# Performance work log

Hardware: AMD Instinct MI355X
Metric: run time of the kernel (lower is better)

Reference implementation:

```python
import math
import jax, jax.numpy as jnp
import numpy as np

MUL = 16          # multiplicity of 0e and 1o in irreps_in/out
DIM = 4 * MUL     # 16 scalars + 16 vectors*3 = 64 channels
DIAMETER = 5.0
STEPS = (1.0, 1.0, 1.0)
NB = 8            # num_radial_basis


def gen_lattice():
    r = DIAMETER / 2
    ax = [jnp.arange(-math.floor(r / s), math.floor(r / s) + 1.0) * s for s in STEPS]
    return jnp.stack(jnp.meshgrid(*ax, indexing='ij'), axis=-1)  # [kx,ky,kz,3]


def radial_emb(r):
    # soft_one_hot_linspace(basis='smooth_finite', cutoff=True)
    values = jnp.linspace(0.0, DIAMETER / 2, NB + 2)[1:-1]
    step = (DIAMETER / 2) / (NB + 1)
    diff = (r[..., None] - values) / step
    den = jnp.maximum(1.0 - diff * diff, 1e-9)  # avoid nan grads outside support
    return jnp.where(jnp.abs(diff) < 1.0, 1.14136 * jnp.exp(2.0 - 1.0 / den), 0.0)


def sph_l01(vec):
    # spherical harmonics l=0,1 with normalize=True, normalization='component'
    n = jnp.linalg.norm(vec, axis=-1, keepdims=True)
    unit = jnp.where(n > 0, vec / jnp.where(n > 0, n, 1.0), 0.0)
    y0 = jnp.ones(vec.shape[:-1] + (1,), vec.dtype)
    return jnp.concatenate([y0, math.sqrt(3.0) * unit], axis=-1)  # [...,4]


def tp_right(w, sh):
    # Right operand of fully-connected tensor product (in x sh -> out):
    # returns per-lattice-point matrix R [L, DIM_in, DIM_out] s.t. TP(x, sh) = x @ R.
    # Paths (uvw): 0e*0e->0e, 0e*1o->1o, 1o*0e->1o, 1o*1o->0e.
    L = w.shape[0]
    W = w.reshape(L, 4, MUL, MUL)      # per-path weights [u, w] (mul_sh = 1)
    y0, y1 = sh[:, 0], sh[:, 1:4]
    a = 1.0 / math.sqrt(2.0 * MUL)     # fan-in: mul_in * mul_sh * 2 paths per output
    eye3 = jnp.eye(3, dtype=w.dtype)
    Rss = a * W[:, 0] * y0[:, None, None]                                            # [L,16,16]
    Rsv = a * jnp.einsum('luw,lm->luwm', W[:, 1], y1).reshape(L, MUL, 3 * MUL)        # CG = identity
    Rvv = a * jnp.einsum('luw,l,mn->lumwn', W[:, 2], y0, eye3).reshape(L, 3 * MUL, 3 * MUL)
    Rvs = (a / math.sqrt(3.0)) * jnp.einsum('luw,lm->lumw', W[:, 3], y1).reshape(L, 3 * MUL, MUL)  # CG = delta/sqrt3
    return jnp.concatenate([jnp.concatenate([Rss, Rsv], -1),
                            jnp.concatenate([Rvs, Rvv], -1)], 1)  # [L,64,64]


def reference(x, linear_weight, weight):
    lattice = gen_lattice()
    emb = radial_emb(jnp.linalg.norm(lattice, axis=-1))   # [kx,ky,kz,NB]
    sh = sph_l01(lattice)                                  # [kx,ky,kz,4]
    # self-connection: irrep-wise Linear with 1/sqrt(fan_in)
    Wl = linear_weight.reshape(2, MUL, MUL) / math.sqrt(MUL)
    xs = x[..., :MUL]
    xv = x[..., MUL:].reshape(x.shape[:-1] + (MUL, 3))
    sc = jnp.concatenate([
        jnp.einsum('...u,uw->...w', xs, Wl[0]),
        jnp.einsum('...um,uw->...wm', xv, Wl[1]).reshape(x.shape[:-1] + (3 * MUL,))], -1)
    # radial-MLP weights -> per-voxel TP kernel
    kx, ky, kz = sh.shape[:3]
    w = (emb.reshape(-1, NB) @ weight) / (kx * ky * kz)    # [L, 4*MUL*MUL]
    k = tp_right(w, sh.reshape(-1, 4)).reshape(kx, ky, kz, DIM, DIM)
    y = jax.lax.conv_general_dilated(x, k, (1, 1, 1), 'SAME',
                                     dimension_numbers=('NXYZC', 'XYZIO', 'NXYZC'))
    return sc + y


def setup_inputs():
    key = jax.random.key(0)
    k1, k2, k3 = jax.random.split(key, 3)
    return {
        'x': jax.random.normal(k1, (2, 40, 40, 40, DIM), jnp.float32),
        'linear_weight': jax.random.normal(k2, (2 * MUL * MUL,), jnp.float32),
        'weight': jax.random.normal(k3, (NB, 4 * MUL * MUL), jnp.float32),
    }
```

## Files before the change

### kernel.cpp

```cpp
#include <hip/hip_runtime.h>
#include <hip/hip_bf16.h>


typedef __bf16 bf16x8 __attribute__((ext_vector_type(8)));
typedef float f32x4 __attribute__((ext_vector_type(4)));

#define COLCH 577
#define COLSTRIDE (COLCH * 16)
#define LDS_BYTES (8 * COLSTRIDE)

__global__ __launch_bounds__(256) void build_k(const float* __restrict__ lw,
                                               const float* __restrict__ wt,
                                               ushort* __restrict__ Kb) {
  int tid = blockIdx.x * 256 + threadIdx.x;
  int j  = tid & 7;
  int o  = (tid >> 3) & 63;
  int kg = (tid >> 9) & 7;
  int l  = tid >> 12;
  int i  = kg * 8 + j;

  int ix = l / 25; int rem = l - ix * 25; int iy = rem / 5; int iz = rem - iy * 5;
  float cx = (float)(ix - 2), cy = (float)(iy - 2), cz = (float)(iz - 2);
  float r = sqrtf(cx * cx + cy * cy + cz * cz);

  float e[8];
  const float step = 2.5f / 9.0f;
  #pragma unroll
  for (int b = 0; b < 8; b++) {
    float diff = (r - (float)(b + 1) * step) / step;
    float den = fmaxf(1.0f - diff * diff, 1e-9f);
    e[b] = (fabsf(diff) < 1.0f) ? 1.14136f * expf(2.0f - 1.0f / den) : 0.0f;
  }
  float inv = (r > 0.0f) ? 1.0f / r : 0.0f;
  const float s3 = 1.7320508075688772f;
  float y1[3] = { s3 * cx * inv, s3 * cy * inv, s3 * cz * inv };
  const float a  = 0.17677669529663687f;
  const float a3 = 0.10206207261596575f;

  auto wElem = [&](int c, int u, int w) -> float {
    const float* p = wt + c * 256 + u * 16 + w;
    float s = 0.f;
    #pragma unroll
    for (int b = 0; b < 8; b++) s += e[b] * p[b * 1024];
    return s * (1.0f / 125.0f);
  };

  float val;
  if (i < 16) {
    if (o < 16) {
      val = a * wElem(0, i, o);
    } else {
      int om = o - 16; int w = om / 3, m = om - 3 * w;
      val = a * wElem(1, i, w) * y1[m];
    }
  } else {
    int im = i - 16; int u = im / 3, m = im - 3 * u;
    if (o < 16) {
      val = a3 * wElem(3, u, o) * y1[m];
    } else {
      int om = o - 16; int w = om / 3, nn = om - 3 * w;
      val = (m == nn) ? a * wElem(2, u, w) : 0.0f;
    }
  }
  if (l == 62) {
    if (i < 16 && o < 16) {
      val += lw[i * 16 + o] * 0.25f;
    } else if (i >= 16 && o >= 16) {
      int im = i - 16, om = o - 16;
      int u = im / 3, m = im - 3 * u;
      int w = om / 3, nn = om - 3 * w;
      if (m == nn) val += lw[256 + u * 16 + w] * 0.25f;
    }
  }
  __hip_bfloat16 h = __float2bfloat16(val);
  Kb[tid] = *(ushort*)&h;
}

__global__ __launch_bounds__(256, 2) void conv_mfma(const float* __restrict__ x,
                                                    const ushort* __restrict__ Kb_,
                                                    float* __restrict__ out) {
  const char* KbB = (const char*)Kb_;
  __shared__ __align__(16) char smem[LDS_BYTES];

  const int tid = threadIdx.x;
  const int lane = tid & 63;
  const int wv = tid >> 6;
  const int g = lane >> 4, ol = lane & 15;

  int bid = blockIdx.x;
  int yg = bid % 5; int t = bid / 5;
  int ox = t % 40; int n = t / 40;
  int y0 = yg * 8;
  int p0 = ((n * 40 + ox) * 40 + y0) * 40;

  int lanebase[5];
  #pragma unroll
  for (int mt = 0; mt < 5; mt++) {
    int r = wv * 80 + mt * 16 + ol;
    int oyr = r / 40, oz = r - oyr * 40;
    lanebase[mt] = g * COLSTRIDE + (oyr * 48 + oz) * 16;
  }
  const int bbase = g * 1024 + ol * 16;

  f32x4 acc[5][4] = {};

  const float* xn = x + (size_t)n * 40 * 40 * 40 * 64;

  for (int dx = 0; dx < 5; dx++) {
    int ix = ox + dx - 2;
    if (ix < 0 || ix >= 40) continue;
    __syncthreads();
    const float* xpl = xn + (size_t)ix * 40 * 40 * 64;
    for (int it = 0; it < 17; it++) {
      int c = it * 256 + tid;
      if (c < 4224) {
        int ch8 = c & 7;
        int rowsrc = c >> 3;
        int yrel = rowsrc / 44;
        int zr = rowsrc - yrel * 44;
        int iy = y0 - 2 + yrel;
        int iz = zr - 2;
        int4 st = make_int4(0, 0, 0, 0);
        if (iy >= 0 && iy < 40 && iz >= 0 && iz < 40) {
          const float* src = xpl + ((size_t)iy * 40 + iz) * 64 + ch8 * 8;
          float4 f0 = ((const float4*)src)[0];
          float4 f1 = ((const float4*)src)[1];
          union { __hip_bfloat16 h[8]; int4 v4; } u;
          u.h[0] = __float2bfloat16(f0.x); u.h[1] = __float2bfloat16(f0.y);
          u.h[2] = __float2bfloat16(f0.z); u.h[3] = __float2bfloat16(f0.w);
          u.h[4] = __float2bfloat16(f1.x); u.h[5] = __float2bfloat16(f1.y);
          u.h[6] = __float2bfloat16(f1.z); u.h[7] = __float2bfloat16(f1.w);
          st = u.v4;
        }
        *(int4*)(smem + ch8 * COLSTRIDE + (yrel * 48 + zr) * 16) = st;
      }
    }
    __syncthreads();

    const char* kbdx = KbB + (size_t)dx * 25 * 8192 + bbase;
    #pragma unroll 1
    for (int dy = 0; dy < 5; dy++) {
      const int dyoff = dy * 48 * 16;
      const char* kbdy = kbdx + dy * 5 * 8192;
      #pragma unroll
      for (int dz = 0; dz < 5; dz++) {
        const int toff = dyoff + dz * 16;
        bf16x8 a[5][2], b[2][4];
        #pragma unroll
        for (int mt = 0; mt < 5; mt++)
          #pragma unroll
          for (int kc = 0; kc < 2; kc++)
            a[mt][kc] = *(const bf16x8*)(smem + lanebase[mt] + kc * (4 * COLSTRIDE) + toff);
        const char* kb = kbdy + dz * 8192;
        #pragma unroll
        for (int kc = 0; kc < 2; kc++)
          #pragma unroll
          for (int nt = 0; nt < 4; nt++)
            b[kc][nt] = *(const bf16x8*)(kb + kc * 4096 + nt * 256);
        #pragma unroll
        for (int kc = 0; kc < 2; kc++)
          #pragma unroll
          for (int nt = 0; nt < 4; nt++)
            #pragma unroll
            for (int mt = 0; mt < 5; mt++)
              acc[mt][nt] = __builtin_amdgcn_mfma_f32_16x16x32_bf16(a[mt][kc], b[kc][nt], acc[mt][nt], 0, 0, 0);
      }
    }
  }

  __syncthreads();
  float* sw = (float*)(smem + wv * (16 * 66 * 4));
  #pragma unroll 1
  for (int mt = 0; mt < 5; mt++) {
    #pragma unroll
    for (int nt = 0; nt < 4; nt++)
      #pragma unroll
      for (int j = 0; j < 4; j++)
        sw[(g * 4 + j) * 66 + nt * 16 + ol] = acc[mt][nt][j];
    float* outb = out + (size_t)(p0 + wv * 80 + mt * 16) * 64;
    #pragma unroll
    for (int i = 0; i < 4; i++) {
      int4 vv = *(int4*)&sw[(i * 4 + g) * 66 + ol * 4];
      ((int4*)outb)[i * 64 + lane] = vv;
    }
  }
}

extern "C" void kernel_launch(void* const* d_in, const int* in_sizes, int n_in,
                              void* d_out, int out_size, void* d_ws, size_t ws_size,
                              hipStream_t stream) {
  const float* x  = (const float*)d_in[0];
  const float* lw = (const float*)d_in[1];
  const float* wt = (const float*)d_in[2];
  float* out = (float*)d_out;
  ushort* Kb = (ushort*)d_ws;

  build_k<<<2000, 256, 0, stream>>>(lw, wt, Kb);
  conv_mfma<<<400, 256, 0, stream>>>(x, Kb, out);
}
```

Baseline: 301.1 us.

## Pre-pad and convert input to bf16 halves, split conv into smaller blocks

A prep kernel now writes a zero-padded bf16 copy of x, split into two 32-channel halves, alongside the fused kernel-weight build. The conv kernel loads slabs straight from this buffer with no bounds checks or fp32 conversion, and loops over channel halves to halve LDS usage. It runs 800 blocks of 128 threads with an XCD-aware block remap. Output is written directly from registers instead of being staged through LDS. The cost is an extra global round trip for the padded bf16 copy and output stores that are less coalesced.

```diff
diff --git a/kernel.cpp b/kernel.cpp
--- a/kernel.cpp
+++ b/kernel.cpp
@@ -5,80 +5,109 @@
 typedef __bf16 bf16x8 __attribute__((ext_vector_type(8)));
 typedef float f32x4 __attribute__((ext_vector_type(4)));
 
-#define COLCH 577
-#define COLSTRIDE (COLCH * 16)
-#define LDS_BYTES (8 * COLSTRIDE)
+#define XP_CHUNKS 1362944
+#define XP_BYTES  (XP_CHUNKS * 16)
+#define COLU 385
+#define COLSTRIDE (COLU * 16)
+#define LDS_BYTES (4 * COLSTRIDE)
 
-__global__ __launch_bounds__(256) void build_k(const float* __restrict__ lw,
-                                               const float* __restrict__ wt,
-                                               ushort* __restrict__ Kb) {
-  int tid = blockIdx.x * 256 + threadIdx.x;
-  int j  = tid & 7;
-  int o  = (tid >> 3) & 63;
-  int kg = (tid >> 9) & 7;
-  int l  = tid >> 12;
-  int i  = kg * 8 + j;
+__global__ __launch_bounds__(256) void prep(const float* __restrict__ x,
+                                            const float* __restrict__ lw,
+                                            const float* __restrict__ wt,
+                                            ushort* __restrict__ xp,
+                                            ushort* __restrict__ Kb) {
+  if (blockIdx.x < 5324) {
+    int u = blockIdx.x * 256 + threadIdx.x;
+    int c8 = u & 3;
+    int v = u >> 2;
+    int zi = v % 44; int w = v / 44;
+    int yi = w % 44; int w2 = w / 44;
+    int h = w2 & 1; int w3 = w2 >> 1;
+    int xi = w3 % 44; int n = w3 / 44;
+    int4 st = make_int4(0, 0, 0, 0);
+    if (xi >= 2 && xi < 42 && yi >= 2 && yi < 42 && zi >= 2 && zi < 42) {
+      const float* src = x + ((((size_t)n * 40 + (xi - 2)) * 40 + (yi - 2)) * 40 + (zi - 2)) * 64
+                           + h * 32 + c8 * 8;
+      float4 f0 = ((const float4*)src)[0];
+      float4 f1 = ((const float4*)src)[1];
+      union { __hip_bfloat16 hh[8]; int4 v4; } uu;
+      uu.hh[0] = __float2bfloat16(f0.x); uu.hh[1] = __float2bfloat16(f0.y);
+      uu.hh[2] = __float2bfloat16(f0.z); uu.hh[3] = __float2bfloat16(f0.w);
+      uu.hh[4] = __float2bfloat16(f1.x); uu.hh[5] = __float2bfloat16(f1.y);
+      uu.hh[6] = __float2bfloat16(f1.z); uu.hh[7] = __float2bfloat16(f1.w);
+      st = uu.v4;
+    }
+    ((int4*)xp)[u] = st;
+  } else {
+    int tid = (blockIdx.x - 5324) * 256 + threadIdx.x;
+    int j  = tid & 7;
+    int o  = (tid >> 3) & 63;
+    int kg = (tid >> 9) & 7;
+    int l  = tid >> 12;
+    int i  = kg * 8 + j;
 
-  int ix = l / 25; int rem = l - ix * 25; int iy = rem / 5; int iz = rem - iy * 5;
-  float cx = (float)(ix - 2), cy = (float)(iy - 2), cz = (float)(iz - 2);
-  float r = sqrtf(cx * cx + cy * cy + cz * cz);
+    int ix = l / 25; int rem = l - ix * 25; int iy = rem / 5; int iz = rem - iy * 5;
+    float cx = (float)(ix - 2), cy = (float)(iy - 2), cz = (float)(iz - 2);
+    float r = sqrtf(cx * cx + cy * cy + cz * cz);
 
-  float e[8];
-  const float step = 2.5f / 9.0f;
-  #pragma unroll
-  for (int b = 0; b < 8; b++) {
-    float diff = (r - (float)(b + 1) * step) / step;
-    float den = fmaxf(1.0f - diff * diff, 1e-9f);
-    e[b] = (fabsf(diff) < 1.0f) ? 1.14136f * expf(2.0f - 1.0f / den) : 0.0f;
+    float e[8];
+    const float step = 2.5f / 9.0f;
+    #pragma unroll
+    for (int b = 0; b < 8; b++) {
+      float diff = (r - (float)(b + 1) * step) / step;
+      float den = fmaxf(1.0f - diff * diff, 1e-9f);
+      e[b] = (fabsf(diff) < 1.0f) ? 1.14136f * expf(2.0f - 1.0f / den) : 0.0f;
+    }
+    float inv = (r > 0.0f) ? 1.0f / r : 0.0f;
+    const float s3 = 1.7320508075688772f;
+    float y1[3] = { s3 * cx * inv, s3 * cy * inv, s3 * cz * inv };
+    const float a  = 0.17677669529663687f;
+    const float a3 = 0.10206207261596575f;
+
+    auto wElem = [&](int c, int u_, int w_) -> float {
+      const float* p = wt + c * 256 + u_ * 16 + w_;
+      float s = 0.f;
+      #pragma unroll
+      for (int b = 0; b < 8; b++) s += e[b] * p[b * 1024];
+      return s * (1.0f / 125.0f);
+    };
+
+    float val;
+    if (i < 16) {
+      if (o < 16) {
+        val = a * wElem(0, i, o);
+      } else {
+        int om = o - 16; int w_ = om / 3, m = om - 3 * w_;
+        val = a * wElem(1, i, w_) * y1[m];
+      }
+    } else {
+      int im = i - 16; int u_ = im / 3, m = im - 3 * u_;
+      if (o < 16) {
+        val = a3 * wElem(3, u_, o) * y1[m];
+      } else {
+        int om = o - 16; int w_ = om / 3, nn = om - 3 * w_;
+        val = (m == nn) ? a * wElem(2, u_, w_) : 0.0f;
+      }
+    }
+    if (l == 62) {
+      if (i < 16 && o < 16) {
+        val += lw[i * 16 + o] * 0.25f;
+      } else if (i >= 16 && o >= 16) {
+        int im = i - 16, om = o - 16;
+        int u_ = im / 3, m = im - 3 * u_;
+        int w_ = om / 3, nn = om - 3 * w_;
+        if (m == nn) val += lw[256 + u_ * 16 + w_] * 0.25f;
+      }
+    }
+    __hip_bfloat16 hv = __float2bfloat16(val);
+    Kb[tid] = *(ushort*)&hv;
   }
-  float inv = (r > 0.0f) ? 1.0f / r : 0.0f;
-  const float s3 = 1.7320508075688772f;
-  float y1[3] = { s3 * cx * inv, s3 * cy * inv, s3 * cz * inv };
-  const float a  = 0.17677669529663687f;
-  const float a3 = 0.10206207261596575f;
-
-  auto wElem = [&](int c, int u, int w) -> float {
-    const float* p = wt + c * 256 + u * 16 + w;
-    float s = 0.f;
-    #pragma unroll
-    for (int b = 0; b < 8; b++) s += e[b] * p[b * 1024];
-    return s * (1.0f / 125.0f);
-  };
-
-  float val;
-  if (i < 16) {
-    if (o < 16) {
-      val = a * wElem(0, i, o);
-    } else {
-      int om = o - 16; int w = om / 3, m = om - 3 * w;
-      val = a * wElem(1, i, w) * y1[m];
-    }
-  } else {
-    int im = i - 16; int u = im / 3, m = im - 3 * u;
-    if (o < 16) {
-      val = a3 * wElem(3, u, o) * y1[m];
-    } else {
-      int om = o - 16; int w = om / 3, nn = om - 3 * w;
-      val = (m == nn) ? a * wElem(2, u, w) : 0.0f;
-    }
-  }
-  if (l == 62) {
-    if (i < 16 && o < 16) {
-      val += lw[i * 16 + o] * 0.25f;
-    } else if (i >= 16 && o >= 16) {
-      int im = i - 16, om = o - 16;
-      int u = im / 3, m = im - 3 * u;
-      int w = om / 3, nn = om - 3 * w;
-      if (m == nn) val += lw[256 + u * 16 + w] * 0.25f;
-    }
-  }
-  __hip_bfloat16 h = __float2bfloat16(val);
-  Kb[tid] = *(ushort*)&h;
 }
 
-__global__ __launch_bounds__(256, 2) void conv_mfma(const float* __restrict__ x,
+__global__ __launch_bounds__(128, 3) void conv_mfma(const ushort* __restrict__ xp_,
                                                     const ushort* __restrict__ Kb_,
                                                     float* __restrict__ out) {
+  const int4* xp4 = (const int4*)xp_;
   const char* KbB = (const char*)Kb_;
   __shared__ __align__(16) char smem[LDS_BYTES];
 
@@ -88,102 +117,71 @@
   const int g = lane >> 4, ol = lane & 15;
 
   int bid = blockIdx.x;
-  int yg = bid % 5; int t = bid / 5;
+  int wg = (bid & 7) * 100 + (bid >> 3);
+  int yg = wg % 10; int t = wg / 10;
   int ox = t % 40; int n = t / 40;
-  int y0 = yg * 8;
+  int y0 = yg * 4;
   int p0 = ((n * 40 + ox) * 40 + y0) * 40;
 
   int lanebase[5];
   #pragma unroll
   for (int mt = 0; mt < 5; mt++) {
     int r = wv * 80 + mt * 16 + ol;
-    int oyr = r / 40, oz = r - oyr * 40;
-    lanebase[mt] = g * COLSTRIDE + (oyr * 48 + oz) * 16;
+    int yo = r / 40, zo = r - yo * 40;
+    lanebase[mt] = g * COLSTRIDE + (yo * 44 + zo) * 16;
   }
-  const int bbase = g * 1024 + ol * 16;
+  const int bb = g * 1024 + ol * 16;
 
   f32x4 acc[5][4] = {};
 
-  const float* xn = x + (size_t)n * 40 * 40 * 40 * 64;
+  for (int h = 0; h < 2; h++) {
+    for (int dx = 0; dx < 5; dx++) {
+      const int4* slab = xp4 + (size_t)((n * 44 + ox + dx) * 2 + h) * 7744 + y0 * 176;
+      int4 v[11];
+      #pragma unroll
+      for (int it = 0; it < 11; it++)
+        v[it] = slab[it * 128 + tid];
+      __syncthreads();
+      #pragma unroll
+      for (int it = 0; it < 11; it++) {
+        int c = it * 128 + tid;
+        *(int4*)(smem + ((c & 3) * COLU + (c >> 2)) * 16) = v[it];
+      }
+      __syncthreads();
 
-  for (int dx = 0; dx < 5; dx++) {
-    int ix = ox + dx - 2;
-    if (ix < 0 || ix >= 40) continue;
-    __syncthreads();
-    const float* xpl = xn + (size_t)ix * 40 * 40 * 64;
-    for (int it = 0; it < 17; it++) {
-      int c = it * 256 + tid;
-      if (c < 4224) {
-        int ch8 = c & 7;
-        int rowsrc = c >> 3;
-        int yrel = rowsrc / 44;
-        int zr = rowsrc - yrel * 44;
-        int iy = y0 - 2 + yrel;
-        int iz = zr - 2;
-        int4 st = make_int4(0, 0, 0, 0);
-        if (iy >= 0 && iy < 40 && iz >= 0 && iz < 40) {
-          const float* src = xpl + ((size_t)iy * 40 + iz) * 64 + ch8 * 8;
-          float4 f0 = ((const float4*)src)[0];
-          float4 f1 = ((const float4*)src)[1];
-          union { __hip_bfloat16 h[8]; int4 v4; } u;
-          u.h[0] = __float2bfloat16(f0.x); u.h[1] = __float2bfloat16(f0.y);
-          u.h[2] = __float2bfloat16(f0.z); u.h[3] = __float2bfloat16(f0.w);
-          u.h[4] = __float2bfloat16(f1.x); u.h[5] = __float2bfloat16(f1.y);
-          u.h[6] = __float2bfloat16(f1.z); u.h[7] = __float2bfloat16(f1.w);
-          st = u.v4;
-        }
-        *(int4*)(smem + ch8 * COLSTRIDE + (yrel * 48 + zr) * 16) = st;
-      }
-    }
-    __syncthreads();
-
-    const char* kbdx = KbB + (size_t)dx * 25 * 8192 + bbase;
-    #pragma unroll 1
-    for (int dy = 0; dy < 5; dy++) {
-      const int dyoff = dy * 48 * 16;
-      const char* kbdy = kbdx + dy * 5 * 8192;
-      #pragma unroll
-      for (int dz = 0; dz < 5; dz++) {
-        const int toff = dyoff + dz * 16;
-        bf16x8 a[5][2], b[2][4];
+      const char* kb0 = KbB + (size_t)dx * 25 * 8192 + h * 4096 + bb;
+      #pragma unroll 1
+      for (int dy = 0; dy < 5; dy++) {
+        const int rowoff = dy * 44 * 16;
+        const char* kby = kb0 + dy * 5 * 8192;
         #pragma unroll
-        for (int mt = 0; mt < 5; mt++)
+        for (int dz = 0; dz < 5; dz++) {
+          bf16x8 a[5], b[4];
           #pragma unroll
-          for (int kc = 0; kc < 2; kc++)
-            a[mt][kc] = *(const bf16x8*)(smem + lanebase[mt] + kc * (4 * COLSTRIDE) + toff);
-        const char* kb = kbdy + dz * 8192;
-        #pragma unroll
-        for (int kc = 0; kc < 2; kc++)
+          for (int mt = 0; mt < 5; mt++)
+            a[mt] = *(const bf16x8*)(smem + lanebase[mt] + rowoff + dz * 16);
           #pragma unroll
           for (int nt = 0; nt < 4; nt++)
-            b[kc][nt] = *(const bf16x8*)(kb + kc * 4096 + nt * 256);
-        #pragma unroll
-        for (int kc = 0; kc < 2; kc++)
+            b[nt] = *(const bf16x8*)(kby + dz * 8192 + nt * 256);
           #pragma unroll
           for (int nt = 0; nt < 4; nt++)
             #pragma unroll
             for (int mt = 0; mt < 5; mt++)
-              acc[mt][nt] = __builtin_amdgcn_mfma_f32_16x16x32_bf16(a[mt][kc], b[kc][nt], acc[mt][nt], 0, 0, 0);
+              acc[mt][nt] = __builtin_amdgcn_mfma_f32_16x16x32_bf16(a[mt], b[nt], acc[mt][nt], 0, 0, 0);
+        }
       }
     }
   }
 
-  __syncthreads();
-  float* sw = (float*)(smem + wv * (16 * 66 * 4));
-  #pragma unroll 1
-  for (int mt = 0; mt < 5; mt++) {
+  #pragma unroll
+  for (int mt = 0; mt < 5; mt++)
     #pragma unroll
     for (int nt = 0; nt < 4; nt++)
       #pragma unroll
-      for (int j = 0; j < 4; j++)
-        sw[(g * 4 + j) * 66 + nt * 16 + ol] = acc[mt][nt][j];
-    float* outb = out + (size_t)(p0 + wv * 80 + mt * 16) * 64;
-    #pragma unroll
-    for (int i = 0; i < 4; i++) {
-      int4 vv = *(int4*)&sw[(i * 4 + g) * 66 + ol * 4];
-      ((int4*)outb)[i * 64 + lane] = vv;
-    }
-  }
+      for (int j = 0; j < 4; j++) {
+        int p = p0 + wv * 80 + mt * 16 + g * 4 + j;
+        out[(size_t)p * 64 + nt * 16 + ol] = acc[mt][nt][j];
+      }
 }
 
 extern "C" void kernel_launch(void* const* d_in, const int* in_sizes, int n_in,
@@ -193,8 +191,9 @@
   const float* lw = (const float*)d_in[1];
   const float* wt = (const float*)d_in[2];
   float* out = (float*)d_out;
-  ushort* Kb = (ushort*)d_ws;
+  ushort* xp = (ushort*)d_ws;
+  ushort* Kb = (ushort*)((char*)d_ws + XP_BYTES);
 
-  build_k<<<2000, 256, 0, stream>>>(lw, wt, Kb);
-  conv_mfma<<<400, 256, 0, stream>>>(x, Kb, out);
+  prep<<<7324, 256, 0, stream>>>(x, lw, wt, xp, Kb);
+  conv_mfma<<<800, 128, 0, stream>>>(xp, Kb, out);
 }
```

Result: faster. 288.8 us (-4.1%).
